# Kernel optimization log

Measured on AMD Instinct MI355X. Metric: run time of the kernel, lower is better.

Reference implementation:

```python
import jax, jax.numpy as jnp
import numpy as np

B, DYN, STAT, U_DIM, N_OBS, H = 4096, 128, 64, 16, 50, 256
HZ = DYN + STAT  # 192
EPS = 1e-5


def setup_inputs() -> dict:
    key = jax.random.key(0)
    ks = jax.random.split(key, 20)
    def lin(k, out_d, in_d):
        s = 1.0 / np.sqrt(in_d)
        kw, kb = jax.random.split(k)
        return (jax.random.uniform(kw, (out_d, in_d), jnp.float32, -s, s),
                jax.random.uniform(kb, (out_d,), jnp.float32, -s, s))
    sel_in = DYN + STAT + 1  # 193
    W1, b1 = lin(ks[0], H, sel_in)
    W2, b2 = lin(ks[1], H, H)
    W3, b3 = lin(ks[2], HZ, H)
    WK, bK = lin(ks[3], DYN * DYN, HZ)
    WL, bL = lin(ks[4], DYN * U_DIM, HZ)
    C = jax.random.normal(ks[5], (N_OBS, DYN), jnp.float32) / np.sqrt(DYN)
    D = jax.random.normal(ks[6], (N_OBS, U_DIM), jnp.float32) / np.sqrt(U_DIM)
    return {
        'z_dyn': jax.random.normal(ks[7], (B, DYN), jnp.float32),
        'z_static': jax.random.normal(ks[8], (B, STAT), jnp.float32),
        'dt': jax.random.uniform(ks[9], (B, 1), jnp.float32),
        'ut': jax.random.normal(ks[10], (B, U_DIM), jnp.float32),
        'W1': W1, 'b1': b1, 'g1': jnp.ones((H,), jnp.float32), 'be1': jnp.zeros((H,), jnp.float32),
        'W2': W2, 'b2': b2, 'g2': jnp.ones((H,), jnp.float32), 'be2': jnp.zeros((H,), jnp.float32),
        'W3': W3, 'b3': b3,
        'WK': WK, 'bK': bK, 'WL': WL, 'bL': bL,
        'C': C, 'D': D,
    }


def _bn(x, g, b):
    # BatchNorm1d in training mode: batch stats, biased variance
    m = jnp.mean(x, axis=0)
    v = jnp.var(x, axis=0)
    return g * (x - m) * jax.lax.rsqrt(v + EPS) + b


def reference(z_dyn, z_static, dt, ut, W1, b1, g1, be1, W2, b2, g2, be2,
              W3, b3, WK, bK, WL, bL, C, D):
    x = jnp.concatenate([z_dyn, z_static, dt], axis=-1)  # (B, 193)
    h = jax.nn.relu(_bn(x @ W1.T + b1, g1, be1))
    h = jax.nn.relu(_bn(h @ W2.T + b2, g2, be2))
    hz = h @ W3.T + b3                                    # (B, HZ)
    Kt = (hz @ WK.T + bK).reshape(-1, DYN, DYN)           # (B, D, D)
    Lt = (hz @ WL.T + bL).reshape(-1, DYN, U_DIM)         # (B, D, U)
    ut_dt = ut * dt
    z_dyn_next = jnp.einsum('bij,bj->bi', Kt, z_dyn) + jnp.einsum('biu,bu->bi', Lt, ut_dt)
    yt = z_dyn_next @ C.T + ut_dt @ D.T                   # (B, n_obs)
    return (z_dyn_next, yt)
```

## Files before the change

kernel.cpp:

```cpp
#include <hip/hip_runtime.h>
#include <stdint.h>

using short8 = __attribute__((ext_vector_type(8))) short;
using f32x4  = __attribute__((ext_vector_type(4))) float;
typedef unsigned short u16;
typedef unsigned int   u32;

#define OFF_X    0u
#define OFF_W1   1835008u
#define OFF_W2   1949696u
#define OFF_W3   2080768u
#define OFF_BM   2179072u
#define OFF_Q    10567680u
#define OFF_P    11878400u
#define OFF_T1   13582336u
#define OFF_T2   17776640u
#define OFF_ST   21970944u
#define WS_NEED  21975040u

__device__ __forceinline__ float b2f(u16 u){ u32 x = ((u32)u)<<16; float f; __builtin_memcpy(&f,&x,4); return f; }
__device__ __forceinline__ u16 f2b(float f){ u32 x; __builtin_memcpy(&x,&f,4); u32 r = (x + 0x7FFFu + ((x>>16)&1u))>>16; return (u16)r; }
__device__ __forceinline__ float u2f(u32 x){ float f; __builtin_memcpy(&f,&x,4); return f; }
__device__ __forceinline__ u32 swz64(u32 row){ return ((row ^ (row>>2)) & 3u) << 4; }
__device__ __forceinline__ u32 swz512(u32 row){ return (row & 7u) << 4; }
__device__ __forceinline__ u32 cvtpk(float lo, float hi){ u32 d; asm("v_cvt_pk_bf16_f32 %0, %1, %2" : "=v"(d) : "v"(lo), "v"(hi)); return d; }

union U16x8 { uint4 u; short8 s; };

__global__ __launch_bounds__(256) void prep_misc(
    const float* __restrict__ z_dyn, const float* __restrict__ z_static,
    const float* __restrict__ dt, const float* __restrict__ ut,
    const float* __restrict__ W1, const float* __restrict__ W2, const float* __restrict__ W3,
    u16* __restrict__ Xb, u16* __restrict__ qg, u16* __restrict__ pg,
    u16* __restrict__ W1b, u16* __restrict__ W2b, u16* __restrict__ W3b)
{
  const int NX = 4096*224, NQ = 4096*160, NP = 4096*16, NW1 = 256*224, NW2 = 256*256, NW3 = 192*256;
  const int total = NX+NQ+NP+NW1+NW2+NW3;
  for (int i = blockIdx.x*256 + threadIdx.x; i < total; i += gridDim.x*256) {
    int idx = i;
    if (idx < NX) {
      int b = idx / 224, k = idx % 224;
      float v = (k < 128) ? z_dyn[b*128+k] : (k < 192 ? z_static[b*64+(k-128)] : (k == 192 ? dt[b] : 0.f));
      Xb[idx] = f2b(v);
    } else if ((idx -= NX) < NQ) {
      int b = idx / 160, c = idx % 160;
      float v = (c < 128) ? z_dyn[b*128+c] : (c < 144 ? ut[b*16+(c-128)]*dt[b] : 0.f);
      qg[idx] = f2b(v);
    } else if ((idx -= NQ) < NP) {
      int b = idx >> 4, c = idx & 15;
      pg[b*208 + 192 + c] = (c == 0) ? (u16)0x3F80 : (u16)0;
    } else if ((idx -= NP) < NW1) {
      int j = idx / 224, k = idx % 224;
      W1b[idx] = f2b(k < 193 ? W1[j*193+k] : 0.f);
    } else if ((idx -= NW1) < NW2) {
      W2b[idx] = f2b(W2[idx]);
    } else { idx -= NW2;
      W3b[idx] = f2b(W3[idx]);
    }
  }
}

__global__ __launch_bounds__(256) void prep_bmat(
    const float* __restrict__ WK, const float* __restrict__ bK,
    const float* __restrict__ WL, const float* __restrict__ bL, u16* __restrict__ Bm)
{
  int i   = blockIdx.x >> 4;
  int kk0 = (blockIdx.x & 15) * 2048 + threadIdx.x * 8;
  int a = kk0 / 160, c = kk0 % 160;
  u16 v[8];
  #pragma unroll
  for (int e = 0; e < 8; ++e) {
    int ce = c + e; float f = 0.f;
    if (ce < 144 && a <= 192) {
      if (a < 192) f = (ce < 128) ? WK[(i*128+ce)*192 + a] : WL[(i*16+(ce-128))*192 + a];
      else         f = (ce < 128) ? bK[i*128+ce]           : bL[i*16+(ce-128)];
    }
    v[e] = f2b(f);
  }
  *(uint4*)(Bm + i*32768 + kk0) = *(uint4*)v;
}

template<int MODE>
__global__ __launch_bounds__(256) void gemm_mlp(
    const u16* __restrict__ Asrc_bf, const float* __restrict__ Asrc_f,
    const u16* __restrict__ Wb, int kstride, int ksteps,
    const float* __restrict__ S1, const float* __restrict__ S2,
    const float* __restrict__ g, const float* __restrict__ be,
    const float* __restrict__ bias,
    float* __restrict__ out_f, u16* __restrict__ out_b)
{
  __shared__ __align__(16) u16 As[2][128*32];
  __shared__ __align__(16) u16 Bs[2][64*32];
  __shared__ float scale_s[256], shift_s[256];
  const int tid = threadIdx.x, lane = tid & 63, wid = tid >> 6;
  const int wr = wid >> 1, wc = wid & 1;
  const int b0 = blockIdx.x * 128, n0 = blockIdx.y * 64;

  if constexpr (MODE >= 1) {
    float m = S1[tid] * (1.f/4096.f);
    float v = S2[tid] * (1.f/4096.f) - m*m;
    float sc = g[tid] * rsqrtf(v + 1e-5f);
    scale_s[tid] = sc; shift_s[tid] = be[tid] - m*sc;
    __syncthreads();
  }

  uint4 arr[2]; uint4 brr;
  auto loadA = [&](int t){
    int k0 = t*32;
    #pragma unroll
    for (int h = 0; h < 2; ++h) {
      int cI = tid + h*256; int row = cI >> 2, j = cI & 3;
      if constexpr (MODE == 0) {
        arr[h] = *(const uint4*)(Asrc_bf + (b0+row)*224 + k0 + j*8);
      } else {
        const float* src = Asrc_f + (b0+row)*256 + k0 + j*8;
        u32 d[4];
        #pragma unroll
        for (int p = 0; p < 4; ++p) {
          int kA = k0 + j*8 + p*2, kB = kA + 1;
          float h0 = fmaxf(0.f, src[p*2]   * scale_s[kA] + shift_s[kA]);
          float h1 = fmaxf(0.f, src[p*2+1] * scale_s[kB] + shift_s[kB]);
          d[p] = cvtpk(h0, h1);
        }
        arr[h] = make_uint4(d[0], d[1], d[2], d[3]);
      }
    }
  };
  auto loadB = [&](int t){
    int k0 = t*32; int col = tid >> 2, j = tid & 3;
    brr = *(const uint4*)(Wb + (n0+col)*kstride + k0 + j*8);
  };
  auto writeAB = [&](int buf){
    #pragma unroll
    for (int h = 0; h < 2; ++h) {
      int cI = tid + h*256; int row = cI >> 2, j = cI & 3;
      *(uint4*)((char*)As[buf] + row*64 + ((j*16) ^ swz64(row))) = arr[h];
    }
    { int col = tid >> 2, j = tid & 3;
      *(uint4*)((char*)Bs[buf] + col*64 + ((j*16) ^ swz64(col))) = brr; }
  };

  f32x4 acc[4][2];
  #pragma unroll
  for (int i = 0; i < 4; ++i)
    #pragma unroll
    for (int j = 0; j < 2; ++j) acc[i][j] = f32x4{0.f,0.f,0.f,0.f};

  loadA(0); loadB(0); writeAB(0);
  __syncthreads();

  for (int t = 0; t < ksteps; ++t) {
    int buf = t & 1;
    if (t + 1 < ksteps) { loadA(t+1); loadB(t+1); }
    short8 af[4], bfr[2];
    #pragma unroll
    for (int mf = 0; mf < 4; ++mf) {
      u32 row = wr*64 + mf*16 + (lane & 15);
      U16x8 u; u.u = *(const uint4*)((const char*)As[buf] + row*64 + ((16*(lane>>4)) ^ swz64(row)));
      af[mf] = u.s;
    }
    #pragma unroll
    for (int nf = 0; nf < 2; ++nf) {
      u32 col = wc*32 + nf*16 + (lane & 15);
      U16x8 u; u.u = *(const uint4*)((const char*)Bs[buf] + col*64 + ((16*(lane>>4)) ^ swz64(col)));
      bfr[nf] = u.s;
    }
    #pragma unroll
    for (int mf = 0; mf < 4; ++mf)
      #pragma unroll
      for (int nf = 0; nf < 2; ++nf)
        acc[mf][nf] = __builtin_amdgcn_mfma_f32_16x16x32_bf16(af[mf], bfr[nf], acc[mf][nf], 0, 0, 0);
    if (t + 1 < ksteps) writeAB(buf ^ 1);
    __syncthreads();
  }

  float bvals[2];
  #pragma unroll
  for (int nf = 0; nf < 2; ++nf) bvals[nf] = bias[n0 + wc*32 + nf*16 + (lane & 15)];
  #pragma unroll
  for (int mf = 0; mf < 4; ++mf)
    #pragma unroll
    for (int nf = 0; nf < 2; ++nf) {
      int colg = n0 + wc*32 + nf*16 + (lane & 15);
      #pragma unroll
      for (int r = 0; r < 4; ++r) {
        int m = b0 + wr*64 + mf*16 + (lane>>4)*4 + r;
        float v = acc[mf][nf][r] + bvals[nf];
        if constexpr (MODE <= 1) out_f[m*256 + colg] = v;
        else                     out_b[m*208 + colg] = f2b(v);
      }
    }
}

__global__ __launch_bounds__(256) void stats_k(const float* __restrict__ t, float* __restrict__ S1, float* __restrict__ S2)
{
  int j = threadIdx.x; int b0 = blockIdx.x * 64;
  float s1 = 0.f, s2 = 0.f;
  for (int r = 0; r < 64; ++r) { float v = t[(b0+r)*256 + j]; s1 += v; s2 += v*v; }
  atomicAdd(&S1[j], s1); atomicAdd(&S2[j], s2);
}

__global__ __launch_bounds__(256) void big_gemm(
    const u16* __restrict__ Bm, const u16* __restrict__ qg, const u16* __restrict__ pg,
    float* __restrict__ zn)
{
  __shared__ __align__(16) u16 q_s[64*256];
  __shared__ __align__(16) u16 b_s[2][128*32];
  const int tid = threadIdx.x, lane = tid & 63, wid = tid >> 6;
  const int wr = wid >> 1, wc = wid & 1;
  const int b0 = blockIdx.x * 64;
  const int kbase = blockIdx.y * 2048;

  for (int cI = tid; cI < 1280; cI += 256) {
    int row = cI / 20, j = cI % 20;
    uint4 v = *(const uint4*)(qg + (b0+row)*160 + j*8);
    *(uint4*)((char*)q_s + row*512 + ((j*16) ^ swz512((u32)row))) = v;
  }

  uint4 r0, r1;
  auto loadB = [&](int t){
    int k0 = kbase + t*32;
    { int col = tid >> 2, j = tid & 3; r0 = *(const uint4*)(Bm + col*32768 + k0 + j*8); }
    { int cI = tid + 256; int col = cI >> 2, j = cI & 3; r1 = *(const uint4*)(Bm + col*32768 + k0 + j*8); }
  };
  auto writeB = [&](int buf){
    { int col = tid >> 2, j = tid & 3; *(uint4*)((char*)b_s[buf] + col*64 + ((j*16) ^ swz64((u32)col))) = r0; }
    { int cI = tid + 256; int col = cI >> 2, j = cI & 3; *(uint4*)((char*)b_s[buf] + col*64 + ((j*16) ^ swz64((u32)col))) = r1; }
  };

  loadB(0); writeB(0);
  __syncthreads();

  f32x4 acc[2][4];
  #pragma unroll
  for (int i = 0; i < 2; ++i)
    #pragma unroll
    for (int j = 0; j < 4; ++j) acc[i][j] = f32x4{0.f,0.f,0.f,0.f};

  int cur_a = -1; float pv[2] = {0.f, 0.f};
  for (int t = 0; t < 64; ++t) {
    int buf = t & 1;
    int k0 = kbase + t*32;
    int a = k0 / 160, c0 = k0 % 160;
    if (t < 63) loadB(t+1);
    if (a != cur_a) { cur_a = a;
      #pragma unroll
      for (int mf = 0; mf < 2; ++mf) {
        int row = wr*32 + mf*16 + (lane & 15);
        pv[mf] = b2f(pg[(b0+row)*208 + a]);
      }
    }
    short8 af[2];
    #pragma unroll
    for (int mf = 0; mf < 2; ++mf) {
      u32 row = wr*32 + mf*16 + (lane & 15);
      uint4 qv = *(const uint4*)((const char*)q_s + row*512 + (((u32)(c0 + 8*(lane>>4))*2u) ^ swz512(row)));
      u32 d[4];
      #pragma unroll
      for (int i2 = 0; i2 < 4; ++i2) {
        u32 qq = (&qv.x)[i2];
        float lo = u2f(qq << 16) * pv[mf];
        float hi = u2f(qq & 0xffff0000u) * pv[mf];
        d[i2] = cvtpk(lo, hi);
      }
      U16x8 u; u.u = make_uint4(d[0], d[1], d[2], d[3]);
      af[mf] = u.s;
    }
    short8 bfr[4];
    #pragma unroll
    for (int nf = 0; nf < 4; ++nf) {
      u32 col = wc*64 + nf*16 + (lane & 15);
      U16x8 u; u.u = *(const uint4*)((const char*)b_s[buf] + col*64 + ((16*(lane>>4)) ^ swz64(col)));
      bfr[nf] = u.s;
    }
    #pragma unroll
    for (int mf = 0; mf < 2; ++mf)
      #pragma unroll
      for (int nf = 0; nf < 4; ++nf)
        acc[mf][nf] = __builtin_amdgcn_mfma_f32_16x16x32_bf16(af[mf], bfr[nf], acc[mf][nf], 0, 0, 0);
    if (t < 63) writeB(buf ^ 1);
    __syncthreads();
  }

  #pragma unroll
  for (int mf = 0; mf < 2; ++mf)
    #pragma unroll
    for (int nf = 0; nf < 4; ++nf) {
      int colg = wc*64 + nf*16 + (lane & 15);
      #pragma unroll
      for (int r = 0; r < 4; ++r) {
        int m = b0 + wr*32 + mf*16 + (lane>>4)*4 + r;
        atomicAdd(&zn[m*128 + colg], acc[mf][nf][r]);
      }
    }
}

__global__ __launch_bounds__(256) void yt_kernel(
    const float* __restrict__ zn, const float* __restrict__ ut, const float* __restrict__ dt,
    const float* __restrict__ C, const float* __restrict__ D, float* __restrict__ yt)
{
  __shared__ float zn_s[32][132];
  __shared__ float C_s[50][132];
  __shared__ float D_s[50][16];
  __shared__ float ud_s[32][16];
  int tid = threadIdx.x; int b0 = blockIdx.x * 32;
  for (int i = tid; i < 32*128; i += 256) { int r = i >> 7, j = i & 127; zn_s[r][j] = zn[(b0+r)*128 + j]; }
  for (int i = tid; i < 50*128; i += 256) { int r = i >> 7, j = i & 127; C_s[r][j] = C[i]; }
  for (int i = tid; i < 50*16;  i += 256) { D_s[i>>4][i&15] = D[i]; }
  for (int i = tid; i < 32*16;  i += 256) { int r = i >> 4, u = i & 15; ud_s[r][u] = ut[(b0+r)*16 + u] * dt[b0+r]; }
  __syncthreads();
  for (int idx = tid; idx < 1600; idx += 256) {
    int o = idx >> 5, r = idx & 31;
    float acc = 0.f;
    #pragma unroll 4
    for (int j = 0; j < 128; ++j) acc += C_s[o][j] * zn_s[r][j];
    #pragma unroll
    for (int u = 0; u < 16; ++u)  acc += D_s[o][u] * ud_s[r][u];
    yt[(b0+r)*50 + o] = acc;
  }
}

extern "C" void kernel_launch(void* const* d_in, const int* in_sizes, int n_in,
                              void* d_out, int out_size, void* d_ws, size_t ws_size,
                              hipStream_t stream) {
  (void)in_sizes; (void)n_in; (void)out_size;
  if (ws_size < (size_t)WS_NEED) return;
  const float* z_dyn = (const float*)d_in[0];
  const float* z_st  = (const float*)d_in[1];
  const float* dt    = (const float*)d_in[2];
  const float* ut    = (const float*)d_in[3];
  const float* W1 = (const float*)d_in[4];  const float* b1 = (const float*)d_in[5];
  const float* g1 = (const float*)d_in[6];  const float* be1 = (const float*)d_in[7];
  const float* W2 = (const float*)d_in[8];  const float* b2 = (const float*)d_in[9];
  const float* g2 = (const float*)d_in[10]; const float* be2 = (const float*)d_in[11];
  const float* W3 = (const float*)d_in[12]; const float* b3 = (const float*)d_in[13];
  const float* WK = (const float*)d_in[14]; const float* bK = (const float*)d_in[15];
  const float* WL = (const float*)d_in[16]; const float* bL = (const float*)d_in[17];
  const float* C  = (const float*)d_in[18]; const float* D  = (const float*)d_in[19];

  char* ws = (char*)d_ws;
  u16* Xb  = (u16*)(ws + OFF_X);
  u16* W1b = (u16*)(ws + OFF_W1);
  u16* W2b = (u16*)(ws + OFF_W2);
  u16* W3b = (u16*)(ws + OFF_W3);
  u16* Bm  = (u16*)(ws + OFF_BM);
  u16* qg  = (u16*)(ws + OFF_Q);
  u16* pg  = (u16*)(ws + OFF_P);
  float* t1 = (float*)(ws + OFF_T1);
  float* t2 = (float*)(ws + OFF_T2);
  float* S1a = (float*)(ws + OFF_ST);
  float* S2a = S1a + 256;
  float* S1b = S1a + 512;
  float* S2b = S1a + 768;

  float* zn = (float*)d_out;
  float* yt = (float*)d_out + 4096*128;

  hipMemsetAsync(d_out, 0, 4096*128*sizeof(float), stream);
  hipMemsetAsync(ws + OFF_ST, 0, 4096, stream);

  prep_misc<<<1024, 256, 0, stream>>>(z_dyn, z_st, dt, ut, W1, W2, W3, Xb, qg, pg, W1b, W2b, W3b);
  prep_bmat<<<2048, 256, 0, stream>>>(WK, bK, WL, bL, Bm);

  gemm_mlp<0><<<dim3(32,4), 256, 0, stream>>>(Xb, nullptr, W1b, 224, 7,
      nullptr, nullptr, nullptr, nullptr, b1, t1, nullptr);
  stats_k<<<64, 256, 0, stream>>>(t1, S1a, S2a);
  gemm_mlp<1><<<dim3(32,4), 256, 0, stream>>>(nullptr, t1, W2b, 256, 8,
      S1a, S2a, g1, be1, b2, t2, nullptr);
  stats_k<<<64, 256, 0, stream>>>(t2, S1b, S2b);
  gemm_mlp<2><<<dim3(32,3), 256, 0, stream>>>(nullptr, t2, W3b, 256, 8,
      S1b, S2b, g2, be2, b3, nullptr, pg);

  big_gemm<<<dim3(64,16), 256, 0, stream>>>(Bm, qg, pg, zn);
  yt_kernel<<<128, 256, 0, stream>>>(zn, ut, dt, C, D, yt);
}
```

Baseline: 165.9 us.

## Load big_gemm B fragments directly to registers, remap blocks, coalesce weight prep

big_gemm stops staging the weight tile through double-buffered LDS and instead prefetches each wave's MFMA B fragments from global memory straight into registers, which removes the per-step __syncthreads. The 1D grid is remapped so that consecutive blocks share the same K slice and reuse it in L2. prep_bmat now reads WK/WL contiguously and scatters bf16 writes, with a memset to zero the padding. The trade-offs are duplicate global B loads across waves (wr), 2-byte scattered stores in prep, and an extra memset.

```diff
diff --git a/kernel.cpp b/kernel.cpp
--- a/kernel.cpp
+++ b/kernel.cpp
@@ -64,20 +64,27 @@
     const float* __restrict__ WK, const float* __restrict__ bK,
     const float* __restrict__ WL, const float* __restrict__ bL, u16* __restrict__ Bm)
 {
-  int i   = blockIdx.x >> 4;
-  int kk0 = (blockIdx.x & 15) * 2048 + threadIdx.x * 8;
-  int a = kk0 / 160, c = kk0 % 160;
-  u16 v[8];
-  #pragma unroll
-  for (int e = 0; e < 8; ++e) {
-    int ce = c + e; float f = 0.f;
-    if (ce < 144 && a <= 192) {
-      if (a < 192) f = (ce < 128) ? WK[(i*128+ce)*192 + a] : WL[(i*16+(ce-128))*192 + a];
-      else         f = (ce < 128) ? bK[i*128+ce]           : bL[i*16+(ce-128)];
-    }
-    v[e] = f2b(f);
-  }
-  *(uint4*)(Bm + i*32768 + kk0) = *(uint4*)v;
+  const int MAIN = 128*144*24;
+  int gid = blockIdx.x*256 + threadIdx.x;
+  if (gid < MAIN) {
+    int aoct = gid % 24;
+    int ce   = (gid / 24) % 144;
+    int i    = gid / (24*144);
+    int a0   = aoct * 8;
+    const float* src = (ce < 128) ? (WK + (i*128+ce)*192 + a0)
+                                  : (WL + (i*16+(ce-128))*192 + a0);
+    u16* dst = Bm + (long)i*32768;
+    #pragma unroll
+    for (int e = 0; e < 8; ++e)
+      dst[(a0+e)*160 + ce] = f2b(src[e]);
+  } else {
+    int g2 = gid - MAIN;
+    if (g2 < 128*144) {
+      int i = g2 / 144, ce = g2 % 144;
+      float v = (ce < 128) ? bK[i*128+ce] : bL[i*16+(ce-128)];
+      Bm[(long)i*32768 + 192*160 + ce] = f2b(v);
+    }
+  }
 }
 
 template<int MODE>
@@ -205,31 +212,28 @@
     float* __restrict__ zn)
 {
   __shared__ __align__(16) u16 q_s[64*256];
-  __shared__ __align__(16) u16 b_s[2][128*32];
   const int tid = threadIdx.x, lane = tid & 63, wid = tid >> 6;
   const int wr = wid >> 1, wc = wid & 1;
-  const int b0 = blockIdx.x * 64;
-  const int kbase = blockIdx.y * 2048;
+  const int lo16 = lane & 15, hi = lane >> 4;
+
+  const int fid  = blockIdx.x;
+  const int orig = (fid & 7) * 128 + (fid >> 3);
+  const int b0    = (orig & 63) * 64;
+  const int kbase = (orig >> 6) * 2048;
 
   for (int cI = tid; cI < 1280; cI += 256) {
     int row = cI / 20, j = cI % 20;
     uint4 v = *(const uint4*)(qg + (b0+row)*160 + j*8);
     *(uint4*)((char*)q_s + row*512 + ((j*16) ^ swz512((u32)row))) = v;
   }
-
-  uint4 r0, r1;
-  auto loadB = [&](int t){
-    int k0 = kbase + t*32;
-    { int col = tid >> 2, j = tid & 3; r0 = *(const uint4*)(Bm + col*32768 + k0 + j*8); }
-    { int cI = tid + 256; int col = cI >> 2, j = cI & 3; r1 = *(const uint4*)(Bm + col*32768 + k0 + j*8); }
-  };
-  auto writeB = [&](int buf){
-    { int col = tid >> 2, j = tid & 3; *(uint4*)((char*)b_s[buf] + col*64 + ((j*16) ^ swz64((u32)col))) = r0; }
-    { int cI = tid + 256; int col = cI >> 2, j = cI & 3; *(uint4*)((char*)b_s[buf] + col*64 + ((j*16) ^ swz64((u32)col))) = r1; }
-  };
-
-  loadB(0); writeB(0);
   __syncthreads();
+
+  const u16* bp0 = Bm + (long)(wc*64 + lo16)*32768 + kbase + hi*8;
+
+  uint4 bcur[4], bnxt[4];
+  #pragma unroll
+  for (int nf = 0; nf < 4; ++nf)
+    bcur[nf] = *(const uint4*)(bp0 + (long)nf*16*32768);
 
   f32x4 acc[2][4];
   #pragma unroll
@@ -239,57 +243,55 @@
 
   int cur_a = -1; float pv[2] = {0.f, 0.f};
   for (int t = 0; t < 64; ++t) {
-    int buf = t & 1;
     int k0 = kbase + t*32;
     int a = k0 / 160, c0 = k0 % 160;
-    if (t < 63) loadB(t+1);
+    if (t < 63) {
+      #pragma unroll
+      for (int nf = 0; nf < 4; ++nf)
+        bnxt[nf] = *(const uint4*)(bp0 + (long)nf*16*32768 + (t+1)*32);
+    }
     if (a != cur_a) { cur_a = a;
       #pragma unroll
       for (int mf = 0; mf < 2; ++mf) {
-        int row = wr*32 + mf*16 + (lane & 15);
+        int row = wr*32 + mf*16 + lo16;
         pv[mf] = b2f(pg[(b0+row)*208 + a]);
       }
     }
     short8 af[2];
     #pragma unroll
     for (int mf = 0; mf < 2; ++mf) {
-      u32 row = wr*32 + mf*16 + (lane & 15);
-      uint4 qv = *(const uint4*)((const char*)q_s + row*512 + (((u32)(c0 + 8*(lane>>4))*2u) ^ swz512(row)));
+      u32 row = (u32)(wr*32 + mf*16 + lo16);
+      uint4 qv = *(const uint4*)((const char*)q_s + row*512 + (((u32)(c0 + 8*hi)*2u) ^ swz512(row)));
       u32 d[4];
       #pragma unroll
       for (int i2 = 0; i2 < 4; ++i2) {
         u32 qq = (&qv.x)[i2];
         float lo = u2f(qq << 16) * pv[mf];
-        float hi = u2f(qq & 0xffff0000u) * pv[mf];
-        d[i2] = cvtpk(lo, hi);
+        float hf = u2f(qq & 0xffff0000u) * pv[mf];
+        d[i2] = cvtpk(lo, hf);
       }
       U16x8 u; u.u = make_uint4(d[0], d[1], d[2], d[3]);
       af[mf] = u.s;
     }
-    short8 bfr[4];
+    #pragma unroll
+    for (int mf = 0; mf < 2; ++mf)
+      #pragma unroll
+      for (int nf = 0; nf < 4; ++nf) {
+        U16x8 u; u.u = bcur[nf];
+        acc[mf][nf] = __builtin_amdgcn_mfma_f32_16x16x32_bf16(af[mf], u.s, acc[mf][nf], 0, 0, 0);
+      }
+    #pragma unroll
+    for (int nf = 0; nf < 4; ++nf) bcur[nf] = bnxt[nf];
+  }
+
+  #pragma unroll
+  for (int mf = 0; mf < 2; ++mf)
     #pragma unroll
     for (int nf = 0; nf < 4; ++nf) {
-      u32 col = wc*64 + nf*16 + (lane & 15);
-      U16x8 u; u.u = *(const uint4*)((const char*)b_s[buf] + col*64 + ((16*(lane>>4)) ^ swz64(col)));
-      bfr[nf] = u.s;
-    }
-    #pragma unroll
-    for (int mf = 0; mf < 2; ++mf)
-      #pragma unroll
-      for (int nf = 0; nf < 4; ++nf)
-        acc[mf][nf] = __builtin_amdgcn_mfma_f32_16x16x32_bf16(af[mf], bfr[nf], acc[mf][nf], 0, 0, 0);
-    if (t < 63) writeB(buf ^ 1);
-    __syncthreads();
-  }
-
-  #pragma unroll
-  for (int mf = 0; mf < 2; ++mf)
-    #pragma unroll
-    for (int nf = 0; nf < 4; ++nf) {
-      int colg = wc*64 + nf*16 + (lane & 15);
+      int colg = wc*64 + nf*16 + lo16;
       #pragma unroll
       for (int r = 0; r < 4; ++r) {
-        int m = b0 + wr*32 + mf*16 + (lane>>4)*4 + r;
+        int m = b0 + wr*32 + mf*16 + hi*4 + r;
         atomicAdd(&zn[m*128 + colg], acc[mf][nf][r]);
       }
     }
@@ -358,9 +360,10 @@
 
   hipMemsetAsync(d_out, 0, 4096*128*sizeof(float), stream);
   hipMemsetAsync(ws + OFF_ST, 0, 4096, stream);
+  hipMemsetAsync(Bm, 0, (size_t)128*32768*sizeof(u16), stream);
 
   prep_misc<<<1024, 256, 0, stream>>>(z_dyn, z_st, dt, ut, W1, W2, W3, Xb, qg, pg, W1b, W2b, W3b);
-  prep_bmat<<<2048, 256, 0, stream>>>(WK, bK, WL, bL, Bm);
+  prep_bmat<<<1800, 256, 0, stream>>>(WK, bK, WL, bL, Bm);
 
   gemm_mlp<0><<<dim3(32,4), 256, 0, stream>>>(Xb, nullptr, W1b, 224, 7,
       nullptr, nullptr, nullptr, nullptr, b1, t1, nullptr);
@@ -371,6 +374,6 @@
   gemm_mlp<2><<<dim3(32,3), 256, 0, stream>>>(nullptr, t2, W3b, 256, 8,
       S1b, S2b, g2, be2, b3, nullptr, pg);
 
-  big_gemm<<<dim3(64,16), 256, 0, stream>>>(Bm, qg, pg, zn);
+  big_gemm<<<1024, 256, 0, stream>>>(Bm, qg, pg, zn);
   yt_kernel<<<128, 256, 0, stream>>>(zn, ut, dt, C, D, yt);
 }
```

Result: slower. 225.5 us (+35.9%).
